# Kernel tuning notes

Hardware: AMD Instinct MI355X
Metric: run time of the kernel (lower is better)

Reference implementation:

```python
import jax, jax.numpy as jnp
import numpy as np

B, S, D, H = 2, 2048, 1024, 16


def setup_inputs() -> dict:
    key = jax.random.key(0)
    kq, kk, kv, kw = jax.random.split(key, 4)
    Q = jax.random.normal(kq, (B, S, D), dtype=jnp.float32)
    K = jax.random.normal(kk, (B, S, D), dtype=jnp.float32)
    V = jax.random.normal(kv, (B, S, D), dtype=jnp.float32)
    Wo = jax.random.normal(kw, (D, D), dtype=jnp.float32) * (1.0 / np.sqrt(D))
    return {"Q": Q, "K": K, "V": V, "Wo": Wo, "num_heads": H}


def reference(Q, K, V, Wo, num_heads):
    b, s, d = Q.shape
    dk = d // num_heads
    # split heads: [B,S,D] -> [B,H,S,dk]
    q = Q.reshape(b, s, num_heads, dk).transpose(0, 2, 1, 3)
    k = K.reshape(b, s, num_heads, dk).transpose(0, 2, 1, 3)
    v = V.reshape(b, s, num_heads, dk).transpose(0, 2, 1, 3)
    scale = 1.0 / jnp.sqrt(jnp.asarray(dk, dtype=q.dtype))
    logits = jnp.einsum('bhqd,bhkd->bhqk', q, k) * scale  # [B,H,S,S]
    probs = jax.nn.softmax(logits, axis=-1).astype(q.dtype)
    o = jnp.einsum('bhqk,bhkd->bhqd', probs, v)  # [B,H,S,dk]
    o = o.transpose(0, 2, 1, 3).reshape(b, s, d)  # concat heads
    # O = einsum('d dkh, ... dkh -> ... d', Wo, scores) == scores @ Wo^T
    return jnp.einsum('dk,bsk->bsd', Wo, o)
```

## Files before the change

kernel.cpp:

```cpp
#include <hip/hip_runtime.h>
#include <hip/hip_bf16.h>

#define B_ 2
#define S_ 2048
#define D_ 1024
#define H_ 16
#define DK_ 64

typedef __hip_bfloat16 bf16;
typedef short v8s __attribute__((ext_vector_type(8)));
typedef short v4s __attribute__((ext_vector_type(4)));
typedef float v4f __attribute__((ext_vector_type(4)));

static __device__ __forceinline__ v4f mfma16(v8s a, v8s b, v4f c) {
  return __builtin_amdgcn_mfma_f32_16x16x32_bf16(a, b, c, 0, 0, 0);
}

static __device__ __forceinline__ void gl2lds16(const void* g, void* l) {
  __builtin_amdgcn_global_load_lds((const __attribute__((address_space(1))) void*)g,
                                   (__attribute__((address_space(3))) void*)l,
                                   16, 0, 0);
}

static __device__ __forceinline__ short f2bf(float x) {
  return (short)__builtin_bit_cast(unsigned short, __float2bfloat16(x));
}

static __device__ __forceinline__ v8s pack8_bf(v4f a, v4f b) {
  v8s r;
  r[0]=f2bf(a[0]); r[1]=f2bf(a[1]); r[2]=f2bf(a[2]); r[3]=f2bf(a[3]);
  r[4]=f2bf(b[0]); r[5]=f2bf(b[1]); r[6]=f2bf(b[2]); r[7]=f2bf(b[3]);
  return r;
}

#define KSTR 72
#define VSTR 40
#define PSTR 40

__global__ __launch_bounds__(256, 2) void attn_kernel(
    const float* __restrict__ Q, const float* __restrict__ K,
    const float* __restrict__ V, bf16* __restrict__ O)
{
  __shared__ __align__(16) bf16 kk[32 * KSTR];
  __shared__ __align__(16) bf16 vv[64 * VSTR];
  __shared__ __align__(16) bf16 pp[4][16 * PSTR];

  const int t = threadIdx.x;
  const int w = t >> 6;
  const int l = t & 63;
  const int quad = l >> 4;
  const int lm = l & 15;

  const int bh = blockIdx.x;
  const int b = bh >> 4;
  const int h = bh & 15;
  const int qbase = blockIdx.y * 64;

  const size_t base = (size_t)b * (S_ * D_) + h * DK_;
  const float* Qb = Q + base;
  const float* Kb = K + base;
  const float* Vb = V + base;

  const float sc = 0.18033688011112042f;

  const int qrow = qbase + w * 16 + lm;
  v8s aq0, aq1;
  {
    const float* qp = Qb + (size_t)qrow * D_ + quad * 8;
    v4f a = *(const v4f*)qp, bq = *(const v4f*)(qp + 4);
    v4f c = *(const v4f*)(qp + 32), d = *(const v4f*)(qp + 36);
#pragma unroll
    for (int i = 0; i < 4; i++) { a[i]*=sc; bq[i]*=sc; c[i]*=sc; d[i]*=sc; }
    aq0 = pack8_bf(a, bq);
    aq1 = pack8_bf(c, d);
  }

  v8s vone;
  {
    const short one_bf = (short)0x3F80, zero = 0;
#pragma unroll
    for (int i = 0; i < 8; i++) vone[i] = (lm == 0) ? one_bf : zero;
  }

  v4f acc0 = {0.f,0.f,0.f,0.f}, acc1 = {0.f,0.f,0.f,0.f};
  v4f acc2 = {0.f,0.f,0.f,0.f}, acc3 = {0.f,0.f,0.f,0.f};
  v4f acc4 = {0.f,0.f,0.f,0.f};

  const int skey = t >> 3;
  const int sseg = t & 7;
  bf16* pw = pp[w];

  v4f kra, krb;
  float vr[8];
  {
    const float* kp = Kb + (size_t)skey * D_ + sseg * 8;
    kra = *(const v4f*)kp; krb = *(const v4f*)(kp + 4);
    const float* vp = Vb + (size_t)skey * D_ + sseg;
#pragma unroll
    for (int i = 0; i < 8; i++) vr[i] = vp[8 * i];
  }

  for (int kb = 0; kb < S_; kb += 32) {
    __syncthreads();
    *(v8s*)(kk + skey * KSTR + sseg * 8) = pack8_bf(kra, krb);
#pragma unroll
    for (int i = 0; i < 8; i++)
      vv[(sseg + 8 * i) * VSTR + skey] = __float2bfloat16(vr[i]);
    __syncthreads();

    if (kb + 32 < S_) {
      const float* kp = Kb + (size_t)(kb + 32 + skey) * D_ + sseg * 8;
      kra = *(const v4f*)kp; krb = *(const v4f*)(kp + 4);
      const float* vp = Vb + (size_t)(kb + 32 + skey) * D_ + sseg;
#pragma unroll
      for (int i = 0; i < 8; i++) vr[i] = vp[8 * i];
    }

    v8s bk00 = *(const v8s*)(kk + lm * KSTR + quad * 8);
    v8s bk01 = *(const v8s*)(kk + lm * KSTR + 32 + quad * 8);
    v8s bk10 = *(const v8s*)(kk + (16 + lm) * KSTR + quad * 8);
    v8s bk11 = *(const v8s*)(kk + (16 + lm) * KSTR + 32 + quad * 8);

    v4f s0 = {0.f,0.f,0.f,0.f}, s1 = {0.f,0.f,0.f,0.f};
    s0 = mfma16(aq0, bk00, s0);
    s0 = mfma16(aq1, bk01, s0);
    s1 = mfma16(aq0, bk10, s1);
    s1 = mfma16(aq1, bk11, s1);

#pragma unroll
    for (int r = 0; r < 4; r++) {
      float p0 = exp2f(s0[r]);
      float p1 = exp2f(s1[r]);
      pw[(quad * 4 + r) * PSTR + lm]      = __float2bfloat16(p0);
      pw[(quad * 4 + r) * PSTR + 16 + lm] = __float2bfloat16(p1);
    }

    asm volatile("" ::: "memory");

    v8s pb = *(const v8s*)(pw + lm * PSTR + quad * 8);
    v8s va0 = *(const v8s*)(vv + (lm)*VSTR + quad * 8);
    v8s va1 = *(const v8s*)(vv + (lm + 16) * VSTR + quad * 8);
    v8s va2 = *(const v8s*)(vv + (lm + 32) * VSTR + quad * 8);
    v8s va3 = *(const v8s*)(vv + (lm + 48) * VSTR + quad * 8);
    acc0 = mfma16(va0, pb, acc0);
    acc1 = mfma16(va1, pb, acc1);
    acc2 = mfma16(va2, pb, acc2);
    acc3 = mfma16(va3, pb, acc3);
    acc4 = mfma16(vone, pb, acc4);
  }

  {
    float lv = __shfl(acc4[0], lm, 64);
    float linv = 1.0f / lv;

    bf16* orow = O + (size_t)(b * S_ + qbase + w * 16 + lm) * D_ + h * DK_;
    v4f av[4] = {acc0, acc1, acc2, acc3};
#pragma unroll
    for (int mt = 0; mt < 4; mt++) {
      v4s pk;
#pragma unroll
      for (int r = 0; r < 4; r++)
        pk[r] = f2bf(av[mt][r] * linv);
      *(v4s*)(orow + mt * 16 + quad * 4) = pk;
    }
  }
}

__global__ __launch_bounds__(256) void wo_cvt_kernel(
    const float* __restrict__ Wo, bf16* __restrict__ Wb)
{
  const int i = (blockIdx.x * 256 + threadIdx.x) * 4;
  v4f a = *(const v4f*)(Wo + i);
  v4s r;
  r[0]=f2bf(a[0]); r[1]=f2bf(a[1]); r[2]=f2bf(a[2]); r[3]=f2bf(a[3]);
  *(v4s*)((short*)Wb + i) = r;
}

__global__ __launch_bounds__(256, 2) void proj_kernel(
    const bf16* __restrict__ A, const bf16* __restrict__ Wo, float* __restrict__ Out)
{
  __shared__ __align__(16) bf16 aa[128 * 32];
  __shared__ __align__(16) bf16 bb[128 * 32];

  const int t = threadIdx.x;
  const int w = t >> 6;
  const int l = t & 63;
  const int quad = l >> 4;
  const int lm = l & 15;

  const int m0 = blockIdx.x * 128;
  const int n0 = blockIdx.y * 128;
  const int wm = (w & 1) * 64;
  const int wn = (w >> 1) * 64;

  v4f acc[4][4];
#pragma unroll
  for (int i = 0; i < 4; i++)
#pragma unroll
    for (int j = 0; j < 4; j++)
      acc[i][j] = {0.f, 0.f, 0.f, 0.f};

  const int srow = t >> 2;
  const int sseg = t & 3;

  for (int k0 = 0; k0 < D_; k0 += 32) {
    __syncthreads();
#pragma unroll
    for (int i = 0; i < 2; i++) {
      const bf16* ga = A  + (size_t)(m0 + srow + 64 * i) * D_ + k0 + sseg * 8;
      const bf16* gb = Wo + (size_t)(n0 + srow + 64 * i) * D_ + k0 + sseg * 8;
      gl2lds16(ga, aa + t * 8 + i * 2048);
      gl2lds16(gb, bb + t * 8 + i * 2048);
    }
    __syncthreads();

    v8s am[4], bn[4];
#pragma unroll
    for (int i = 0; i < 4; i++) {
      am[i] = *(const v8s*)(aa + (wm + i * 16 + lm) * 32 + quad * 8);
      bn[i] = *(const v8s*)(bb + (wn + i * 16 + lm) * 32 + quad * 8);
    }
#pragma unroll
    for (int mi = 0; mi < 4; mi++)
#pragma unroll
      for (int ni = 0; ni < 4; ni++)
        acc[mi][ni] = mfma16(am[mi], bn[ni], acc[mi][ni]);
  }

#pragma unroll
  for (int mi = 0; mi < 4; mi++) {
#pragma unroll
    for (int r = 0; r < 4; r++) {
      const int row = m0 + wm + mi * 16 + quad * 4 + r;
      float* orow = Out + (size_t)row * D_ + n0 + wn + lm;
#pragma unroll
      for (int ni = 0; ni < 4; ni++)
        orow[ni * 16] = acc[mi][ni][r];
    }
  }
}

extern "C" void kernel_launch(void* const* d_in, const int* in_sizes, int n_in,
                              void* d_out, int out_size, void* d_ws, size_t ws_size,
                              hipStream_t stream) {
  (void)in_sizes; (void)n_in; (void)out_size; (void)ws_size;
  const float* Q  = (const float*)d_in[0];
  const float* K  = (const float*)d_in[1];
  const float* V  = (const float*)d_in[2];
  const float* Wo = (const float*)d_in[3];
  float* out = (float*)d_out;
  bf16* ows  = (bf16*)d_ws;
  bf16* wo_b = ows + (size_t)(B_ * S_) * D_;

  wo_cvt_kernel<<<dim3((D_ * D_) / 1024), 256, 0, stream>>>(Wo, wo_b);
  attn_kernel<<<dim3(B_ * H_, S_ / 64), 256, 0, stream>>>(Q, K, V, ows);
  proj_kernel<<<dim3((B_ * S_) / 128, D_ / 128), 256, 0, stream>>>(ows, wo_b, out);
}
```

Before: 196.5 us.

## Pre-convert K/V to bf16 head-major layouts and rewrite attention with 32x32 MFMA

Adds pre-pass kernels that convert K to bf16 in head-major order and transpose V into a bf16 [bh,d,s] layout. The attention kernel then streams these with direct global-to-LDS loads, double-buffered with XOR-swizzled LDS, and uses 32x32x16 MFMA with 128 queries per block. P is shuffled between registers instead of staged through LDS, the row sum is accumulated on the ALU, and the output is staged through LDS for coalesced stores. The projection GEMM switches to 64x128 tiles with double-buffered loads. The cost is extra launches and extra global traffic for the converted copies.

New measurement: 200.1 us. About the same (+1.8%).

```diff
diff --git a/kernel.cpp b/kernel.cpp
--- a/kernel.cpp
+++ b/kernel.cpp
@@ -11,39 +11,204 @@
 typedef short v8s __attribute__((ext_vector_type(8)));
 typedef short v4s __attribute__((ext_vector_type(4)));
 typedef float v4f __attribute__((ext_vector_type(4)));
+typedef float v16f __attribute__((ext_vector_type(16)));
+typedef int   v4i __attribute__((ext_vector_type(4)));
 
 static __device__ __forceinline__ v4f mfma16(v8s a, v8s b, v4f c) {
   return __builtin_amdgcn_mfma_f32_16x16x32_bf16(a, b, c, 0, 0, 0);
 }
-
+static __device__ __forceinline__ v16f mfma32(v8s a, v8s b, v16f c) {
+  return __builtin_amdgcn_mfma_f32_32x32x16_bf16(a, b, c, 0, 0, 0);
+}
 static __device__ __forceinline__ void gl2lds16(const void* g, void* l) {
   __builtin_amdgcn_global_load_lds((const __attribute__((address_space(1))) void*)g,
                                    (__attribute__((address_space(3))) void*)l,
                                    16, 0, 0);
 }
-
-static __device__ __forceinline__ short f2bf(float x) {
-  return (short)__builtin_bit_cast(unsigned short, __float2bfloat16(x));
-}
-
-static __device__ __forceinline__ v8s pack8_bf(v4f a, v4f b) {
+static __device__ __forceinline__ unsigned short bfb(float x) {
+  return __builtin_bit_cast(unsigned short, __float2bfloat16(x));
+}
+static __device__ __forceinline__ short f2bf(float x) { return (short)bfb(x); }
+static __device__ __forceinline__ int pk2(float lo, float hi) {
+  return (int)(((unsigned)bfb(hi) << 16) | (unsigned)bfb(lo));
+}
+
+__global__ __launch_bounds__(256) void cvt_k_kernel(const float* __restrict__ K,
+                                                    bf16* __restrict__ Kb) {
+  const int idx = blockIdx.x * 256 + threadIdx.x;
+  const int seg = idx & 7;
+  const int rest = idx >> 3;
+  const int h = rest & 15;
+  const int bs = rest >> 4;
+  const float* src = K + (size_t)bs * D_ + h * 64 + seg * 8;
+  v4f x = *(const v4f*)src, y = *(const v4f*)(src + 4);
   v8s r;
+  r[0]=f2bf(x[0]); r[1]=f2bf(x[1]); r[2]=f2bf(x[2]); r[3]=f2bf(x[3]);
+  r[4]=f2bf(y[0]); r[5]=f2bf(y[1]); r[6]=f2bf(y[2]); r[7]=f2bf(y[3]);
+  const int b = bs >> 11, s = bs & 2047;
+  *(v8s*)(Kb + ((size_t)(b * H_ + h) * S_ + s) * DK_ + seg * 8) = r;
+}
+
+__global__ __launch_bounds__(256) void tv_kernel(const float* __restrict__ V,
+                                                 bf16* __restrict__ Vt) {
+  __shared__ __align__(16) bf16 td[64 * 72];
+  const int t = threadIdx.x;
+  const int bh = blockIdx.x, b = bh >> 4, h = bh & 15;
+  const int s0 = blockIdx.y * 64;
+  const int srow = t >> 2;
+  const int cs = t & 3;
+  const float* vp = V + (size_t)(b * S_ + s0 + srow) * D_ + h * 64 + cs * 16;
+#pragma unroll
+  for (int j = 0; j < 4; j++) {
+    v4f x = *(const v4f*)(vp + j * 4);
+#pragma unroll
+    for (int jj = 0; jj < 4; jj++)
+      td[(cs * 16 + j * 4 + jj) * 72 + srow] = __float2bfloat16(x[jj]);
+  }
+  __syncthreads();
+  const int d = t >> 2, sseg = t & 3;
+#pragma unroll
+  for (int j = 0; j < 2; j++) {
+    v8s val = *(const v8s*)(td + d * 72 + sseg * 16 + j * 8);
+    *(v8s*)(Vt + ((size_t)bh * DK_ + d) * S_ + s0 + sseg * 16 + j * 8) = val;
+  }
+}
+
+__global__ __launch_bounds__(256) void cvt_wo_kernel(const float* __restrict__ Wo,
+                                                     bf16* __restrict__ Wb) {
+  const int i = (blockIdx.x * 256 + threadIdx.x) * 4;
+  v4f a = *(const v4f*)(Wo + i);
+  v4s r;
   r[0]=f2bf(a[0]); r[1]=f2bf(a[1]); r[2]=f2bf(a[2]); r[3]=f2bf(a[3]);
-  r[4]=f2bf(b[0]); r[5]=f2bf(b[1]); r[6]=f2bf(b[2]); r[7]=f2bf(b[3]);
-  return r;
-}
-
-#define KSTR 72
-#define VSTR 40
-#define PSTR 40
-
-__global__ __launch_bounds__(256, 2) void attn_kernel(
-    const float* __restrict__ Q, const float* __restrict__ K,
-    const float* __restrict__ V, bf16* __restrict__ O)
+  *(v4s*)((short*)Wb + i) = r;
+}
+
+__global__ __launch_bounds__(256, 2) void attn2_kernel(
+    const float* __restrict__ Q, const bf16* __restrict__ Kb,
+    const bf16* __restrict__ Vt, bf16* __restrict__ Ow)
 {
-  __shared__ __align__(16) bf16 kk[32 * KSTR];
-  __shared__ __align__(16) bf16 vv[64 * VSTR];
-  __shared__ __align__(16) bf16 pp[4][16 * PSTR];
+  __shared__ __align__(16) bf16 kk[2][32 * 64];
+  __shared__ __align__(16) bf16 vv[2][64 * 32];
+  __shared__ __align__(16) bf16 ep[4][32 * 72];
+
+  const int t = threadIdx.x;
+  const int w = t >> 6;
+  const int l = t & 63;
+  const int h2 = l >> 5;
+  const int ln = l & 31;
+
+  const int bh = blockIdx.x;
+  const int b = bh >> 4, h = bh & 15;
+  const int qbase = blockIdx.y * 128 + w * 32;
+
+  const bf16* Kbh = Kb + (size_t)bh * (S_ * DK_);
+  const bf16* Vbh = Vt + (size_t)bh * (DK_ * S_);
+
+  const int krow = t >> 3, ksrc_seg = (t & 7) ^ (krow & 7);
+  const int vrow = t >> 2, vsrc_seg = (t & 3) ^ (vrow & 3);
+
+  const float sc = 0.18033688011112042f;
+  v8s bq[4];
+  {
+    const float* qp = Q + ((size_t)b * S_ + qbase + ln) * D_ + h * DK_ + h2 * 8;
+#pragma unroll
+    for (int c = 0; c < 4; c++) {
+      v4f x = *(const v4f*)(qp + c * 16);
+      v4f y = *(const v4f*)(qp + c * 16 + 4);
+      v8s r;
+      r[0]=f2bf(x[0]*sc); r[1]=f2bf(x[1]*sc); r[2]=f2bf(x[2]*sc); r[3]=f2bf(x[3]*sc);
+      r[4]=f2bf(y[0]*sc); r[5]=f2bf(y[1]*sc); r[6]=f2bf(y[2]*sc); r[7]=f2bf(y[3]*sc);
+      bq[c] = r;
+    }
+  }
+
+  v16f accA, accB;
+#pragma unroll
+  for (int r = 0; r < 16; r++) { accA[r] = 0.f; accB[r] = 0.f; }
+  float lpart = 0.f;
+
+  gl2lds16(Kbh + (size_t)krow * DK_ + ksrc_seg * 8, &kk[0][t * 8]);
+  gl2lds16(Vbh + (size_t)vrow * S_ + vsrc_seg * 8, &vv[0][t * 8]);
+
+  int it = 0;
+  for (int kb = 0; kb < S_; kb += 32, it ^= 1) {
+    __syncthreads();
+    if (kb + 32 < S_) {
+      gl2lds16(Kbh + (size_t)(kb + 32 + krow) * DK_ + ksrc_seg * 8, &kk[it ^ 1][t * 8]);
+      gl2lds16(Vbh + (size_t)vrow * S_ + (kb + 32) + vsrc_seg * 8, &vv[it ^ 1][t * 8]);
+    }
+    const bf16* kc_ = kk[it];
+    const bf16* vc_ = vv[it];
+
+    v16f s;
+#pragma unroll
+    for (int r = 0; r < 16; r++) s[r] = 0.f;
+#pragma unroll
+    for (int c = 0; c < 4; c++) {
+      const int sd = 2 * c + h2;
+      v8s ak = *(const v8s*)(kc_ + ln * 64 + ((sd ^ (ln & 7)) * 8));
+      s = mfma32(ak, bq[c], s);
+    }
+
+    float p[16];
+#pragma unroll
+    for (int r = 0; r < 16; r++) p[r] = exp2f(s[r]);
+    float su = 0.f;
+#pragma unroll
+    for (int r = 0; r < 16; r++) su += p[r];
+    lpart += su;
+
+    int Pk[8], Sw[8];
+#pragma unroll
+    for (int g = 0; g < 8; g++) Pk[g] = pk2(p[2 * g], p[2 * g + 1]);
+#pragma unroll
+    for (int g = 0; g < 8; g++) Sw[g] = __shfl_xor(Pk[g], 32);
+
+    v4i b0i, b1i;
+    b0i[0] = h2 ? Sw[2] : Pk[0];  b0i[1] = h2 ? Sw[3] : Pk[1];
+    b0i[2] = h2 ? Pk[2] : Sw[0];  b0i[3] = h2 ? Pk[3] : Sw[1];
+    b1i[0] = h2 ? Sw[6] : Pk[4];  b1i[1] = h2 ? Sw[7] : Pk[5];
+    b1i[2] = h2 ? Pk[6] : Sw[4];  b1i[3] = h2 ? Pk[7] : Sw[5];
+    v8s pb0 = __builtin_bit_cast(v8s, b0i);
+    v8s pb1 = __builtin_bit_cast(v8s, b1i);
+
+#pragma unroll
+    for (int kc = 0; kc < 2; kc++) {
+      const int sk = 2 * kc + h2;
+      const int dA = ln;
+      const int dB = 32 + ln;
+      v8s avA = *(const v8s*)(vc_ + dA * 32 + ((sk ^ (dA & 3)) * 8));
+      v8s avB = *(const v8s*)(vc_ + dB * 32 + ((sk ^ (dB & 3)) * 8));
+      accA = mfma32(avA, kc ? pb1 : pb0, accA);
+      accB = mfma32(avB, kc ? pb1 : pb0, accB);
+    }
+  }
+
+  const float linv = 1.0f / (lpart + __shfl_xor(lpart, 32));
+  bf16* epw = ep[w];
+#pragma unroll
+  for (int r = 0; r < 16; r++) {
+    const int dr = (r & 3) + 8 * (r >> 2) + 4 * h2;
+    epw[ln * 72 + dr]      = __float2bfloat16(accA[r] * linv);
+    epw[ln * 72 + 32 + dr] = __float2bfloat16(accB[r] * linv);
+  }
+  __syncthreads();
+#pragma unroll
+  for (int i = 0; i < 4; i++) {
+    const int flat = i * 64 + l;
+    const int qr = flat >> 3, seg = flat & 7;
+    v8s val = *(const v8s*)(epw + qr * 72 + seg * 8);
+    const int srow = qbase - w * 32 + w * 32 + qr;
+    *(v8s*)(Ow + ((size_t)b * S_ + qbase + qr) * D_ + h * DK_ + seg * 8) = val;
+    (void)srow;
+  }
+}
+
+__global__ __launch_bounds__(256, 2) void proj2_kernel(
+    const bf16* __restrict__ A, const bf16* __restrict__ Wo, float* __restrict__ Out)
+{
+  __shared__ __align__(16) bf16 aa[2][64 * 32];
+  __shared__ __align__(16) bf16 bb[2][128 * 32];
 
   const int t = threadIdx.x;
   const int w = t >> 6;
@@ -51,184 +216,58 @@
   const int quad = l >> 4;
   const int lm = l & 15;
 
-  const int bh = blockIdx.x;
-  const int b = bh >> 4;
-  const int h = bh & 15;
-  const int qbase = blockIdx.y * 64;
-
-  const size_t base = (size_t)b * (S_ * D_) + h * DK_;
-  const float* Qb = Q + base;
-  const float* Kb = K + base;
-  const float* Vb = V + base;
-
-  const float sc = 0.18033688011112042f;
-
-  const int qrow = qbase + w * 16 + lm;
-  v8s aq0, aq1;
-  {
-    const float* qp = Qb + (size_t)qrow * D_ + quad * 8;
-    v4f a = *(const v4f*)qp, bq = *(const v4f*)(qp + 4);
-    v4f c = *(const v4f*)(qp + 32), d = *(const v4f*)(qp + 36);
-#pragma unroll
-    for (int i = 0; i < 4; i++) { a[i]*=sc; bq[i]*=sc; c[i]*=sc; d[i]*=sc; }
-    aq0 = pack8_bf(a, bq);
-    aq1 = pack8_bf(c, d);
-  }
-
-  v8s vone;
-  {
-    const short one_bf = (short)0x3F80, zero = 0;
-#pragma unroll
-    for (int i = 0; i < 8; i++) vone[i] = (lm == 0) ? one_bf : zero;
-  }
-
-  v4f acc0 = {0.f,0.f,0.f,0.f}, acc1 = {0.f,0.f,0.f,0.f};
-  v4f acc2 = {0.f,0.f,0.f,0.f}, acc3 = {0.f,0.f,0.f,0.f};
-  v4f acc4 = {0.f,0.f,0.f,0.f};
-
-  const int skey = t >> 3;
-  const int sseg = t & 7;
-  bf16* pw = pp[w];
-
-  v4f kra, krb;
-  float vr[8];
-  {
-    const float* kp = Kb + (size_t)skey * D_ + sseg * 8;
-    kra = *(const v4f*)kp; krb = *(const v4f*)(kp + 4);
-    const float* vp = Vb + (size_t)skey * D_ + sseg;
-#pragma unroll
-    for (int i = 0; i < 8; i++) vr[i] = vp[8 * i];
-  }
-
-  for (int kb = 0; kb < S_; kb += 32) {
-    __syncthreads();
-    *(v8s*)(kk + skey * KSTR + sseg * 8) = pack8_bf(kra, krb);
-#pragma unroll
-    for (int i = 0; i < 8; i++)
-      vv[(sseg + 8 * i) * VSTR + skey] = __float2bfloat16(vr[i]);
-    __syncthreads();
-
-    if (kb + 32 < S_) {
-      const float* kp = Kb + (size_t)(kb + 32 + skey) * D_ + sseg * 8;
-      kra = *(const v4f*)kp; krb = *(const v4f*)(kp + 4);
-      const float* vp = Vb + (size_t)(kb + 32 + skey) * D_ + sseg;
-#pragma unroll
-      for (int i = 0; i < 8; i++) vr[i] = vp[8 * i];
-    }
-
-    v8s bk00 = *(const v8s*)(kk + lm * KSTR + quad * 8);
-    v8s bk01 = *(const v8s*)(kk + lm * KSTR + 32 + quad * 8);
-    v8s bk10 = *(const v8s*)(kk + (16 + lm) * KSTR + quad * 8);
-    v8s bk11 = *(const v8s*)(kk + (16 + lm) * KSTR + 32 + quad * 8);
-
-    v4f s0 = {0.f,0.f,0.f,0.f}, s1 = {0.f,0.f,0.f,0.f};
-    s0 = mfma16(aq0, bk00, s0);
-    s0 = mfma16(aq1, bk01, s0);
-    s1 = mfma16(aq0, bk10, s1);
-    s1 = mfma16(aq1, bk11, s1);
-
-#pragma unroll
-    for (int r = 0; r < 4; r++) {
-      float p0 = exp2f(s0[r]);
-      float p1 = exp2f(s1[r]);
-      pw[(quad * 4 + r) * PSTR + lm]      = __float2bfloat16(p0);
-      pw[(quad * 4 + r) * PSTR + 16 + lm] = __float2bfloat16(p1);
-    }
-
-    asm volatile("" ::: "memory");
-
-    v8s pb = *(const v8s*)(pw + lm * PSTR + quad * 8);
-    v8s va0 = *(const v8s*)(vv + (lm)*VSTR + quad * 8);
-    v8s va1 = *(const v8s*)(vv + (lm + 16) * VSTR + quad * 8);
-    v8s va2 = *(const v8s*)(vv + (lm + 32) * VSTR + quad * 8);
-    v8s va3 = *(const v8s*)(vv + (lm + 48) * VSTR + quad * 8);
-    acc0 = mfma16(va0, pb, acc0);
-    acc1 = mfma16(va1, pb, acc1);
-    acc2 = mfma16(va2, pb, acc2);
-    acc3 = mfma16(va3, pb, acc3);
-    acc4 = mfma16(vone, pb, acc4);
-  }
-
-  {
-    float lv = __shfl(acc4[0], lm, 64);
-    float linv = 1.0f / lv;
-
-    bf16* orow = O + (size_t)(b * S_ + qbase + w * 16 + lm) * D_ + h * DK_;
-    v4f av[4] = {acc0, acc1, acc2, acc3};
-#pragma unroll
-    for (int mt = 0; mt < 4; mt++) {
-      v4s pk;
-#pragma unroll
-      for (int r = 0; r < 4; r++)
-        pk[r] = f2bf(av[mt][r] * linv);
-      *(v4s*)(orow + mt * 16 + quad * 4) = pk;
-    }
-  }
-}
-
-__global__ __launch_bounds__(256) void wo_cvt_kernel(
-    const float* __restrict__ Wo, bf16* __restrict__ Wb)
-{
-  const int i = (blockIdx.x * 256 + threadIdx.x) * 4;
-  v4f a = *(const v4f*)(Wo + i);
-  v4s r;
-  r[0]=f2bf(a[0]); r[1]=f2bf(a[1]); r[2]=f2bf(a[2]); r[3]=f2bf(a[3]);
-  *(v4s*)((short*)Wb + i) = r;
-}
-
-__global__ __launch_bounds__(256, 2) void proj_kernel(
-    const bf16* __restrict__ A, const bf16* __restrict__ Wo, float* __restrict__ Out)
-{
-  __shared__ __align__(16) bf16 aa[128 * 32];
-  __shared__ __align__(16) bf16 bb[128 * 32];
-
-  const int t = threadIdx.x;
-  const int w = t >> 6;
-  const int l = t & 63;
-  const int quad = l >> 4;
-  const int lm = l & 15;
-
-  const int m0 = blockIdx.x * 128;
+  const int m0 = blockIdx.x * 64;
   const int n0 = blockIdx.y * 128;
-  const int wm = (w & 1) * 64;
+  const int wm = (w & 1) * 32;
   const int wn = (w >> 1) * 64;
 
-  v4f acc[4][4];
-#pragma unroll
-  for (int i = 0; i < 4; i++)
+  v4f acc[2][4];
+#pragma unroll
+  for (int i = 0; i < 2; i++)
 #pragma unroll
     for (int j = 0; j < 4; j++)
       acc[i][j] = {0.f, 0.f, 0.f, 0.f};
 
-  const int srow = t >> 2;
-  const int sseg = t & 3;
-
-  for (int k0 = 0; k0 < D_; k0 += 32) {
+  const int arow = t >> 2, aseg = t & 3;
+
+  gl2lds16(A + (size_t)(m0 + arow) * D_ + aseg * 8, &aa[0][t * 8]);
+#pragma unroll
+  for (int j = 0; j < 2; j++) {
+    const int flat = j * 256 + t;
+    gl2lds16(Wo + (size_t)(n0 + (flat >> 2)) * D_ + (flat & 3) * 8, &bb[0][flat * 8]);
+  }
+
+  int it = 0;
+  for (int k0 = 0; k0 < D_; k0 += 32, it ^= 1) {
     __syncthreads();
-#pragma unroll
-    for (int i = 0; i < 2; i++) {
-      const bf16* ga = A  + (size_t)(m0 + srow + 64 * i) * D_ + k0 + sseg * 8;
-      const bf16* gb = Wo + (size_t)(n0 + srow + 64 * i) * D_ + k0 + sseg * 8;
-      gl2lds16(ga, aa + t * 8 + i * 2048);
-      gl2lds16(gb, bb + t * 8 + i * 2048);
-    }
-    __syncthreads();
-
-    v8s am[4], bn[4];
-#pragma unroll
-    for (int i = 0; i < 4; i++) {
-      am[i] = *(const v8s*)(aa + (wm + i * 16 + lm) * 32 + quad * 8);
-      bn[i] = *(const v8s*)(bb + (wn + i * 16 + lm) * 32 + quad * 8);
-    }
-#pragma unroll
-    for (int mi = 0; mi < 4; mi++)
+    if (k0 + 32 < D_) {
+      gl2lds16(A + (size_t)(m0 + arow) * D_ + (k0 + 32) + aseg * 8, &aa[it ^ 1][t * 8]);
+#pragma unroll
+      for (int j = 0; j < 2; j++) {
+        const int flat = j * 256 + t;
+        gl2lds16(Wo + (size_t)(n0 + (flat >> 2)) * D_ + (k0 + 32) + (flat & 3) * 8,
+                 &bb[it ^ 1][flat * 8]);
+      }
+    }
+    const bf16* ac = aa[it];
+    const bf16* bc = bb[it];
+
+    v8s am[2], bn[4];
+#pragma unroll
+    for (int i = 0; i < 2; i++)
+      am[i] = *(const v8s*)(ac + (wm + i * 16 + lm) * 32 + quad * 8);
+#pragma unroll
+    for (int i = 0; i < 4; i++)
+      bn[i] = *(const v8s*)(bc + (wn + i * 16 + lm) * 32 + quad * 8);
+#pragma unroll
+    for (int mi = 0; mi < 2; mi++)
 #pragma unroll
       for (int ni = 0; ni < 4; ni++)
         acc[mi][ni] = mfma16(am[mi], bn[ni], acc[mi][ni]);
   }
 
 #pragma unroll
-  for (int mi = 0; mi < 4; mi++) {
+  for (int mi = 0; mi < 2; mi++) {
 #pragma unroll
     for (int r = 0; r < 4; r++) {
       const int row = m0 + wm + mi * 16 + quad * 4 + r;
@@ -249,10 +288,15 @@
   const float* V  = (const float*)d_in[2];
   const float* Wo = (const float*)d_in[3];
   float* out = (float*)d_out;
-  bf16* ows  = (bf16*)d_ws;
-  bf16* wo_b = ows + (size_t)(B_ * S_) * D_;
-
-  wo_cvt_kernel<<<dim3((D_ * D_) / 1024), 256, 0, stream>>>(Wo, wo_b);
-  attn_kernel<<<dim3(B_ * H_, S_ / 64), 256, 0, stream>>>(Q, K, V, ows);
-  proj_kernel<<<dim3((B_ * S_) / 128, D_ / 128), 256, 0, stream>>>(ows, wo_b, out);
-}
+
+  bf16* kb   = (bf16*)d_ws;
+  bf16* vt   = kb + (size_t)4 * 1024 * 1024;
+  bf16* ows  = vt + (size_t)4 * 1024 * 1024;
+  bf16* wo_b = ows + (size_t)4 * 1024 * 1024;
+
+  cvt_k_kernel <<<dim3(2048),     256, 0, stream>>>(K, kb);
+  tv_kernel    <<<dim3(32, 32),   256, 0, stream>>>(V, vt);
+  cvt_wo_kernel<<<dim3(1024),     256, 0, stream>>>(Wo, wo_b);
+  attn2_kernel <<<dim3(32, 16),   256, 0, stream>>>(Q, kb, vt, ows);
+  proj2_kernel <<<dim3(64, 8),    256, 0, stream>>>(ows, wo_b, out);
+}
```
